# Kernel tuning notes

Hardware: AMD Instinct MI355X
Metric: run time of the kernel (lower is better)

The kernel has to match this reference:

```python
import jax, jax.numpy as jnp
import numpy as np

D = 3  # interpolation dimensionality (trilinear)


def nd_corners(d):
    # corner offsets of the d-dim unit hypercube: [1, 2^d, d] int32
    xi = [jnp.arange(2, dtype=jnp.int32) for _ in range(d)]
    return jnp.stack(jnp.meshgrid(*xi, indexing='ij'), -1).reshape(1, 2 ** d, d)


def setup_inputs() -> dict:
    key = jax.random.key(0)
    k1, k2 = jax.random.split(key)
    input = jax.random.normal(k1, (16, 128, 128, 128), dtype=jnp.float32)
    # normalized coords in [-1, 1]
    coords = jax.random.uniform(k2, (1000000, 3), dtype=jnp.float32) * 2.0 - 1.0
    return {"input": input, "coords": coords}


def reference(input, coords):
    d = D
    grid_shape = jnp.asarray(input.shape[-d:], dtype=coords.dtype)  # [d]
    # _unnormalize: map [-1, 1] -> grid coords
    c = (coords + 1.0) / 2.0 * (grid_shape - 1.0)
    S = c.shape[:-1]
    c = c.reshape(-1, 1, d)                      # [N, 1, d]
    corners = nd_corners(d)                       # [1, 2^d, d]
    floor = jnp.floor(c)
    # weights_fn: |x - floor(x) + i - 1|, product over dims -> [N, 2^d]
    weights = jnp.abs(c - floor + corners.astype(c.dtype) - 1.0).prod(-1)
    # index_fn + nearest clamp
    index = floor.astype(jnp.int32) + corners     # [N, 2^d, d]
    high = jnp.asarray(input.shape[-d:], dtype=jnp.int32)
    index = jnp.clip(index, 0, high - 1)
    # gather corner values: input[..., i0, i1, i2] -> [C, N, 2^d]
    values = input[..., index[..., 0], index[..., 1], index[..., 2]]
    out = (weights * values).sum(-1)              # [C, N]
    return out.reshape(*input.shape[:-d], *S)
```

## Files before the change

kernel.cpp:

```cpp
#include <hip/hip_runtime.h>


#define GD   128
#define NCH  16
constexpr int VOX = GD * GD * GD;

__device__ __forceinline__ unsigned short f2bf_rne(float f) {
    unsigned u = __builtin_bit_cast(unsigned, f);
    u = u + 0x7fffu + ((u >> 16) & 1u);
    return (unsigned short)(u >> 16);
}

__global__ __launch_bounds__(256) void transpose_half_k(const float* __restrict__ in,
                                                        uint4* __restrict__ ws) {
    int s = blockIdx.x * 256 + threadIdx.x;
    int z = s & (GD - 1);

    float a[NCH];
#pragma unroll
    for (int c = 0; c < NCH; ++c)
        a[c] = __builtin_nontemporal_load(in + (size_t)c * VOX + s);

    unsigned w[8];
#pragma unroll
    for (int k = 0; k < 8; ++k)
        w[k] = (unsigned)f2bf_rne(a[2 * k + 0]) | ((unsigned)f2bf_rne(a[2 * k + 1]) << 16);

    uint4 lo = make_uint4(w[0], w[1], w[2], w[3]);
    uint4 hi = make_uint4(w[4], w[5], w[6], w[7]);

    uint4* o = ws + (size_t)s * 4;
    o[0] = lo;
    o[1] = hi;
    if (z > 0) {
        uint4* p = ws + (size_t)(s - 1) * 4;
        p[2] = lo;
        p[3] = hi;
    }
    if (z == GD - 1) {
        o[2] = lo;
        o[3] = hi;
    }
}

__global__ __launch_bounds__(256) void interp_pair_k(const uint4* __restrict__ ws,
                                                     const float* __restrict__ coords,
                                                     float* __restrict__ out, int N) {
    int n = blockIdx.x * 256 + threadIdx.x;
    if (n >= N) return;

    float cx = (coords[3 * n + 0] + 1.0f) * 0.5f * (float)(GD - 1);
    float cy = (coords[3 * n + 1] + 1.0f) * 0.5f * (float)(GD - 1);
    float cz = (coords[3 * n + 2] + 1.0f) * 0.5f * (float)(GD - 1);

    float fx = floorf(cx), fy = floorf(cy), fz = floorf(cz);
    float tx = cx - fx, ty = cy - fy, tz = cz - fz;
    int ix = (int)fx, iy = (int)fy, iz = (int)fz;

    int ix0 = min(max(ix,     0), GD - 1), ix1 = min(max(ix + 1, 0), GD - 1);
    int iy0 = min(max(iy,     0), GD - 1), iy1 = min(max(iy + 1, 0), GD - 1);
    int iz0 = min(max(iz,     0), GD - 1);

    float wx0 = 1.0f - tx, wx1 = tx;
    float wy0 = 1.0f - ty, wy1 = ty;
    float wz0 = 1.0f - tz, wz1 = tz;

    const uint4* p0 = ws + ((size_t)(ix0 * GD + iy0) * GD + iz0) * 4;
    const uint4* p1 = ws + ((size_t)(ix0 * GD + iy1) * GD + iz0) * 4;
    const uint4* p2 = ws + ((size_t)(ix1 * GD + iy0) * GD + iz0) * 4;
    const uint4* p3 = ws + ((size_t)(ix1 * GD + iy1) * GD + iz0) * 4;

    uint4 q[16];
#pragma unroll
    for (int j = 0; j < 4; ++j) {
        q[0 + j]  = p0[j];
        q[4 + j]  = p1[j];
        q[8 + j]  = p2[j];
        q[12 + j] = p3[j];
    }

    float wxy[4] = { wx0 * wy0, wx0 * wy1, wx1 * wy0, wx1 * wy1 };

    float acc[NCH];
#pragma unroll
    for (int c = 0; c < NCH; ++c) acc[c] = 0.0f;

#pragma unroll
    for (int r = 0; r < 4; ++r) {
        unsigned u0[8] = { q[4 * r + 0].x, q[4 * r + 0].y, q[4 * r + 0].z, q[4 * r + 0].w,
                           q[4 * r + 1].x, q[4 * r + 1].y, q[4 * r + 1].z, q[4 * r + 1].w };
        unsigned u1[8] = { q[4 * r + 2].x, q[4 * r + 2].y, q[4 * r + 2].z, q[4 * r + 2].w,
                           q[4 * r + 3].x, q[4 * r + 3].y, q[4 * r + 3].z, q[4 * r + 3].w };
        float wxyr = wxy[r];
#pragma unroll
        for (int k = 0; k < 8; ++k) {
            float z0lo = __builtin_bit_cast(float, u0[k] << 16);
            float z0hi = __builtin_bit_cast(float, u0[k] & 0xffff0000u);
            float z1lo = __builtin_bit_cast(float, u1[k] << 16);
            float z1hi = __builtin_bit_cast(float, u1[k] & 0xffff0000u);
            acc[2 * k + 0] += wxyr * (wz0 * z0lo + wz1 * z1lo);
            acc[2 * k + 1] += wxyr * (wz0 * z0hi + wz1 * z1hi);
        }
    }

#pragma unroll
    for (int c = 0; c < NCH; ++c)
        __builtin_nontemporal_store(acc[c], out + (size_t)c * N + n);
}

__global__ __launch_bounds__(256) void interp_direct_k(const float* __restrict__ in,
                                                       const float* __restrict__ coords,
                                                       float* __restrict__ out, int N) {
    int n = blockIdx.x * 256 + threadIdx.x;
    if (n >= N) return;
    float cx = (coords[3 * n + 0] + 1.0f) * 0.5f * (float)(GD - 1);
    float cy = (coords[3 * n + 1] + 1.0f) * 0.5f * (float)(GD - 1);
    float cz = (coords[3 * n + 2] + 1.0f) * 0.5f * (float)(GD - 1);
    float fx = floorf(cx), fy = floorf(cy), fz = floorf(cz);
    float tx = cx - fx, ty = cy - fy, tz = cz - fz;
    int ix = (int)fx, iy = (int)fy, iz = (int)fz;
    int ix0 = min(max(ix, 0), GD - 1), ix1 = min(max(ix + 1, 0), GD - 1);
    int iy0 = min(max(iy, 0), GD - 1), iy1 = min(max(iy + 1, 0), GD - 1);
    int iz0 = min(max(iz, 0), GD - 1), iz1 = min(max(iz + 1, 0), GD - 1);
    float wx0 = 1.0f - tx, wx1 = tx, wy0 = 1.0f - ty, wy1 = ty, wz0 = 1.0f - tz, wz1 = tz;
    int o000 = (ix0 * GD + iy0) * GD + iz0, o001 = (ix0 * GD + iy0) * GD + iz1;
    int o010 = (ix0 * GD + iy1) * GD + iz0, o011 = (ix0 * GD + iy1) * GD + iz1;
    int o100 = (ix1 * GD + iy0) * GD + iz0, o101 = (ix1 * GD + iy0) * GD + iz1;
    int o110 = (ix1 * GD + iy1) * GD + iz0, o111 = (ix1 * GD + iy1) * GD + iz1;
    float w000 = wx0 * wy0 * wz0, w001 = wx0 * wy0 * wz1;
    float w010 = wx0 * wy1 * wz0, w011 = wx0 * wy1 * wz1;
    float w100 = wx1 * wy0 * wz0, w101 = wx1 * wy0 * wz1;
    float w110 = wx1 * wy1 * wz0, w111 = wx1 * wy1 * wz1;
#pragma unroll
    for (int c = 0; c < NCH; ++c) {
        const float* g = in + (size_t)c * VOX;
        float acc = w000 * g[o000] + w001 * g[o001] + w010 * g[o010] + w011 * g[o011]
                  + w100 * g[o100] + w101 * g[o101] + w110 * g[o110] + w111 * g[o111];
        out[(size_t)c * N + n] = acc;
    }
}

extern "C" void kernel_launch(void* const* d_in, const int* in_sizes, int n_in,
                              void* d_out, int out_size, void* d_ws, size_t ws_size,
                              hipStream_t stream) {
    const float* input  = (const float*)d_in[0];
    const float* coords = (const float*)d_in[1];
    float* out = (float*)d_out;
    int N = in_sizes[1] / 3;
    int nb = (N + 255) / 256;

    size_t need = (size_t)VOX * 64;
    if (ws_size >= need) {
        transpose_half_k<<<VOX / 256, 256, 0, stream>>>(input, (uint4*)d_ws);
        interp_pair_k<<<nb, 256, 0, stream>>>((const uint4*)d_ws, coords, out, N);
    } else {
        interp_direct_k<<<nb, 256, 0, stream>>>(input, coords, out, N);
    }
}
```

Measured before the change: 312.0 us.

## Pack 2x2 yz corner quads per voxel to halve gather requests

Result: slower. 412.6 us (+32.3%).

```diff
diff --git a/kernel.cpp b/kernel.cpp
--- a/kernel.cpp
+++ b/kernel.cpp
@@ -9,6 +9,96 @@
     unsigned u = __builtin_bit_cast(unsigned, f);
     u = u + 0x7fffu + ((u >> 16) & 1u);
     return (unsigned short)(u >> 16);
+}
+
+__global__ __launch_bounds__(256) void transpose_quad_k(const float* __restrict__ in,
+                                                        uint4* __restrict__ ws) {
+    int s = blockIdx.x * 256 + threadIdx.x;
+    int z = s & (GD - 1);
+    int y = (s >> 7) & (GD - 1);
+
+    float a[NCH];
+#pragma unroll
+    for (int c = 0; c < NCH; ++c)
+        a[c] = __builtin_nontemporal_load(in + (size_t)c * VOX + s);
+
+    unsigned w[8];
+#pragma unroll
+    for (int k = 0; k < 8; ++k)
+        w[k] = (unsigned)f2bf_rne(a[2 * k + 0]) | ((unsigned)f2bf_rne(a[2 * k + 1]) << 16);
+
+    uint4 lo = make_uint4(w[0], w[1], w[2], w[3]);
+    uint4 hi = make_uint4(w[4], w[5], w[6], w[7]);
+
+    uint4* o = ws + (size_t)s * 8;
+    o[0] = lo; o[1] = hi;
+    if (z > 0)          { uint4* p = ws + (size_t)(s - 1) * 8;      p[2] = lo; p[3] = hi; }
+    if (y > 0)          { uint4* p = ws + (size_t)(s - GD) * 8;     p[4] = lo; p[5] = hi; }
+    if (y > 0 && z > 0) { uint4* p = ws + (size_t)(s - GD - 1) * 8; p[6] = lo; p[7] = hi; }
+    if (z == GD - 1)              { o[2] = lo; o[3] = hi; }
+    if (y == GD - 1)              { o[4] = lo; o[5] = hi; }
+    if (y == GD - 1 && z > 0)     { uint4* p = ws + (size_t)(s - 1) * 8;  p[6] = lo; p[7] = hi; }
+    if (z == GD - 1 && y > 0)     { uint4* p = ws + (size_t)(s - GD) * 8; p[6] = lo; p[7] = hi; }
+    if (y == GD - 1 && z == GD - 1) { o[6] = lo; o[7] = hi; }
+}
+
+__global__ __launch_bounds__(256) void interp_quad_k(const uint4* __restrict__ ws,
+                                                     const float* __restrict__ coords,
+                                                     float* __restrict__ out, int N) {
+    int n = blockIdx.x * 256 + threadIdx.x;
+    if (n >= N) return;
+
+    float cx = (coords[3 * n + 0] + 1.0f) * 0.5f * (float)(GD - 1);
+    float cy = (coords[3 * n + 1] + 1.0f) * 0.5f * (float)(GD - 1);
+    float cz = (coords[3 * n + 2] + 1.0f) * 0.5f * (float)(GD - 1);
+
+    float fx = floorf(cx), fy = floorf(cy), fz = floorf(cz);
+    float tx = cx - fx, ty = cy - fy, tz = cz - fz;
+    int ix = (int)fx, iy = (int)fy, iz = (int)fz;
+
+    int ix0 = min(max(ix,     0), GD - 1), ix1 = min(max(ix + 1, 0), GD - 1);
+    int iy0 = min(max(iy,     0), GD - 1);
+    int iz0 = min(max(iz,     0), GD - 1);
+
+    float wx0 = 1.0f - tx, wx1 = tx;
+    float wy0 = 1.0f - ty, wy1 = ty;
+    float wz0 = 1.0f - tz, wz1 = tz;
+
+    const uint4* pA = ws + ((size_t)(ix0 * GD + iy0) * GD + iz0) * 8;
+    const uint4* pB = ws + ((size_t)(ix1 * GD + iy0) * GD + iz0) * 8;
+
+    uint4 q[16];
+#pragma unroll
+    for (int j = 0; j < 8; ++j) { q[j] = pA[j]; q[8 + j] = pB[j]; }
+
+    float wyz[4] = { wy0 * wz0, wy0 * wz1, wy1 * wz0, wy1 * wz1 };
+    float wxc[2] = { wx0, wx1 };
+
+    float acc[NCH];
+#pragma unroll
+    for (int c = 0; c < NCH; ++c) acc[c] = 0.0f;
+
+#pragma unroll
+    for (int xc = 0; xc < 2; ++xc) {
+#pragma unroll
+        for (int sl = 0; sl < 4; ++sl) {
+            const uint4 qa = q[xc * 8 + sl * 2 + 0];
+            const uint4 qb = q[xc * 8 + sl * 2 + 1];
+            unsigned u[8] = { qa.x, qa.y, qa.z, qa.w, qb.x, qb.y, qb.z, qb.w };
+            float wv = wxc[xc] * wyz[sl];
+#pragma unroll
+            for (int k = 0; k < 8; ++k) {
+                float vlo = __builtin_bit_cast(float, u[k] << 16);
+                float vhi = __builtin_bit_cast(float, u[k] & 0xffff0000u);
+                acc[2 * k + 0] += wv * vlo;
+                acc[2 * k + 1] += wv * vhi;
+            }
+        }
+    }
+
+#pragma unroll
+    for (int c = 0; c < NCH; ++c)
+        __builtin_nontemporal_store(acc[c], out + (size_t)c * N + n);
 }
 
 __global__ __launch_bounds__(256) void transpose_half_k(const float* __restrict__ in,
@@ -149,8 +239,12 @@
     int N = in_sizes[1] / 3;
     int nb = (N + 255) / 256;
 
-    size_t need = (size_t)VOX * 64;
-    if (ws_size >= need) {
+    size_t need_quad = (size_t)VOX * 128;
+    size_t need_pair = (size_t)VOX * 64;
+    if (ws_size >= need_quad) {
+        transpose_quad_k<<<VOX / 256, 256, 0, stream>>>(input, (uint4*)d_ws);
+        interp_quad_k<<<nb, 256, 0, stream>>>((const uint4*)d_ws, coords, out, N);
+    } else if (ws_size >= need_pair) {
         transpose_half_k<<<VOX / 256, 256, 0, stream>>>(input, (uint4*)d_ws);
         interp_pair_k<<<nb, 256, 0, stream>>>((const uint4*)d_ws, coords, out, N);
     } else {
```
